# Performance work log

Measured on AMD Instinct MI355X. Metric: run time of the kernel, lower is better.

The kernel has to match this reference:

```python
import jax, jax.numpy as jnp
import numpy as np

B = 8          # batch
RES = 64       # resolution (H = W)
DIM = 512      # channels
HEADS = 8
HD = DIM // HEADS   # 64
HSP, WSP = RES, 8   # idx=0: H_sp=resolution, W_sp=split_size
NH, NW = RES // HSP, RES // WSP   # windows per axis


def setup_inputs() -> dict:
    key = jax.random.key(0)
    k1, k2, k3 = jax.random.split(key, 3)
    qkv = jax.random.normal(k1, (3, B, RES * RES, DIM), dtype=jnp.float32)
    lepe_w = jax.random.normal(k2, (DIM, 1, 3, 3), dtype=jnp.float32) * 0.1
    lepe_b = jax.random.normal(k3, (DIM,), dtype=jnp.float32) * 0.1
    return {"qkv": qkv, "lepe_w": lepe_w, "lepe_b": lepe_b}


def _to_windows(t):
    # [B, L, C] row-major -> [B*NH*NW, HSP*WSP, C]; equivalent to the
    # block-diagonal flex_attention mask grouping (y//H_sp, x//W_sp).
    t = t.reshape(B, NH, HSP, NW, WSP, DIM)
    return t.transpose(0, 1, 3, 2, 4, 5).reshape(B * NH * NW, HSP * WSP, DIM)


def _from_windows(t):
    t = t.reshape(B, NH, NW, HSP, WSP, DIM).transpose(0, 1, 3, 2, 4, 5)
    return t.reshape(B, RES * RES, DIM)


def reference(qkv, lepe_w, lepe_b):
    q, k, v = qkv[0], qkv[1], qkv[2]            # each [B, L, C]
    qw, kw, vw = _to_windows(q), _to_windows(k), _to_windows(v)

    # LePE: depthwise 3x3 conv on v laid out per-window as [n, C, HSP, WSP]
    vimg = vw.transpose(0, 2, 1).reshape(-1, DIM, HSP, WSP)
    lepe = jax.lax.conv_general_dilated(
        vimg, lepe_w, window_strides=(1, 1), padding='SAME',
        dimension_numbers=('NCHW', 'OIHW', 'NCHW'), feature_group_count=DIM)
    lepe = lepe + lepe_b[None, :, None, None]
    lepe = lepe.reshape(-1, DIM, HSP * WSP).transpose(0, 2, 1)  # [n, T, C]

    def split_heads(t):
        return t.reshape(t.shape[0], t.shape[1], HEADS, HD)

    qh, kh, vh, lh = map(split_heads, (qw, kw, vw, lepe))
    scale = 1.0 / np.sqrt(HD).astype(np.float32)  # flex_attention default scale
    scores = jnp.einsum('wqhd,wkhd->whqk', qh, kh) * scale
    attn = jax.nn.softmax(scores, axis=-1)
    out = jnp.einsum('whqk,wkhd->wqhd', attn, vh) + lh   # [n, T, H, hd]
    out = out.reshape(out.shape[0], out.shape[1], DIM)
    return _from_windows(out)
```

## Files before the change

kernel.cpp:

```cpp
#include <hip/hip_runtime.h>
#include <hip/hip_bf16.h>

#define DIMV 512
#define HDV  64
#define VSTR 520
#define VT_BASE 65536
#define SMEM_B (VT_BASE + 64 * VSTR * 2)

typedef __bf16 bf16x8_t __attribute__((ext_vector_type(8)));
typedef float f32x4_t __attribute__((ext_vector_type(4)));

union Frag { bf16x8_t v; unsigned short u[8]; unsigned int w[4]; uint2 d[2]; uint4 q; };

__device__ __forceinline__ unsigned short f2bf(float f) {
  return __builtin_bit_cast(unsigned short, (__bf16)f);
}
__device__ __forceinline__ float bf2f(unsigned int h) {
  return __builtin_bit_cast(float, h << 16);
}

__global__ __launch_bounds__(1024, 1)
void lepe_attn_kernel(const float* __restrict__ qkv,
                      const float* __restrict__ lw,
                      const float* __restrict__ lb,
                      float* __restrict__ out)
{
  __shared__ __align__(16) unsigned char smem[SMEM_B];

  const int head = blockIdx.x & 7;
  const int win  = blockIdx.x >> 3;
  const int bat  = win >> 3;
  const int nw   = win & 7;

  const int tid  = threadIdx.x;
  const int wave = tid >> 6, lane = tid & 63;
  const int l15  = lane & 15, g = lane >> 4;

  const float* qptr = qkv;
  const float* kptr = qkv + 16777216;
  const float* vptr = qkv + 33554432;
  const int rowbase = bat * 4096;

  auto growf = [&](int tok) -> size_t {
    return ((size_t)(rowbase + ((tok >> 3) << 6) + (nw << 3) + (tok & 7))) * DIMV
           + head * HDV;
  };

  const int s_t = tid >> 4;
  const int s_c = (tid & 15) * 4;
  const size_t TSTRIDE = 262144;

  const float* kg = kptr + growf(s_t) + s_c;
  const float* vg = vptr + growf(s_t) + s_c;
  const int kwbase = s_t * 128 + ((s_c * 2) ^ ((s_t & 7) << 4));

  float4 kin[8], vin[8];
  #pragma unroll
  for (int j = 0; j < 8; ++j) kin[j] = *(const float4*)(kg + (size_t)j * TSTRIDE);
  #pragma unroll
  for (int j = 0; j < 8; ++j) vin[j] = *(const float4*)(vg + (size_t)j * TSTRIDE);

  unsigned short* vt = (unsigned short*)(smem + VT_BASE);
  #pragma unroll
  for (int j = 0; j < 8; ++j) {
    uint2 kp;
    kp.x = (unsigned)f2bf(kin[j].x) | ((unsigned)f2bf(kin[j].y) << 16);
    kp.y = (unsigned)f2bf(kin[j].z) | ((unsigned)f2bf(kin[j].w) << 16);
    *(uint2*)(smem + kwbase + j * 8192) = kp;
    int t = s_t + 64 * j;
    vt[(s_c + 0) * VSTR + t] = f2bf(vin[j].x);
    vt[(s_c + 1) * VSTR + t] = f2bf(vin[j].y);
    vt[(s_c + 2) * VSTR + t] = f2bf(vin[j].z);
    vt[(s_c + 3) * VSTR + t] = f2bf(vin[j].w);
  }

  const float QSC = 0.1803368801f;
  const int qbase = wave * 32;
  Frag qf[2][2];
  #pragma unroll
  for (int qi = 0; qi < 2; ++qi) {
    const float* qp = qptr + growf(qbase + qi * 16 + l15);
    #pragma unroll
    for (int kc = 0; kc < 2; ++kc) {
      float4 f0 = *(const float4*)(qp + kc * 32 + 8 * g);
      float4 f1 = *(const float4*)(qp + kc * 32 + 8 * g + 4);
      qf[qi][kc].u[0] = f2bf(f0.x * QSC); qf[qi][kc].u[1] = f2bf(f0.y * QSC);
      qf[qi][kc].u[2] = f2bf(f0.z * QSC); qf[qi][kc].u[3] = f2bf(f0.w * QSC);
      qf[qi][kc].u[4] = f2bf(f1.x * QSC); qf[qi][kc].u[5] = f2bf(f1.y * QSC);
      qf[qi][kc].u[6] = f2bf(f1.z * QSC); qf[qi][kc].u[7] = f2bf(f1.w * QSC);
    }
  }

  __syncthreads();

  const f32x4_t zero4 = {0.f, 0.f, 0.f, 0.f};
  f32x4_t ot[4][2];
  #pragma unroll
  for (int di = 0; di < 4; ++di)
    #pragma unroll
    for (int qi = 0; qi < 2; ++qi) ot[di][qi] = zero4;
  float lsum[2] = {0.f, 0.f};

  const int ksw = (l15 & 7) << 4;
  #pragma unroll 4
  for (int kt = 0; kt < 16; ++kt) {
    Frag kf[2][2];
    #pragma unroll
    for (int ki = 0; ki < 2; ++ki) {
      const unsigned char* rowp = smem + (kt * 32 + ki * 16 + l15) * 128;
      #pragma unroll
      for (int kc = 0; kc < 2; ++kc)
        kf[ki][kc].q = *(const uint4*)(rowp + ((kc * 64 + g * 16) ^ ksw));
    }

    f32x4_t st[2][2];
    #pragma unroll
    for (int ki = 0; ki < 2; ++ki)
      #pragma unroll
      for (int qi = 0; qi < 2; ++qi) st[ki][qi] = zero4;

    __builtin_amdgcn_s_setprio(1);
    #pragma unroll
    for (int kc = 0; kc < 2; ++kc)
      #pragma unroll
      for (int ki = 0; ki < 2; ++ki)
        #pragma unroll
        for (int qi = 0; qi < 2; ++qi)
          st[ki][qi] = __builtin_amdgcn_mfma_f32_16x16x32_bf16(
              kf[ki][kc].v, qf[qi][kc].v, st[ki][qi], 0, 0, 0);
    __builtin_amdgcn_s_setprio(0);

    #pragma unroll
    for (int ki = 0; ki < 2; ++ki)
      #pragma unroll
      for (int qi = 0; qi < 2; ++qi) {
        f32x4_t s = st[ki][qi];
        #pragma unroll
        for (int r = 0; r < 4; ++r) {
          float p = __builtin_amdgcn_exp2f(s[r]);
          s[r] = p;
          lsum[qi] += p;
        }
        st[ki][qi] = s;
      }

    Frag vf[4];
    #pragma unroll
    for (int di = 0; di < 4; ++di) {
      const unsigned char* p = smem + VT_BASE + (di * 16 + l15) * (VSTR * 2)
                               + kt * 64 + 8 * g;
      vf[di].d[0] = *(const uint2*)(p);
      vf[di].d[1] = *(const uint2*)(p + 32);
    }

    __builtin_amdgcn_s_setprio(1);
    #pragma unroll
    for (int qi = 0; qi < 2; ++qi) {
      Frag pb;
      #pragma unroll
      for (int r = 0; r < 4; ++r) {
        pb.u[r]     = f2bf(st[0][qi][r]);
        pb.u[4 + r] = f2bf(st[1][qi][r]);
      }
      #pragma unroll
      for (int di = 0; di < 4; ++di)
        ot[di][qi] = __builtin_amdgcn_mfma_f32_16x16x32_bf16(
            vf[di].v, pb.v, ot[di][qi], 0, 0, 0);
    }
    __builtin_amdgcn_s_setprio(0);
  }

  float rl[2];
  #pragma unroll
  for (int qi = 0; qi < 2; ++qi) {
    float s = lsum[qi];
    s += __shfl_xor(s, 16, 64);
    s += __shfl_xor(s, 32, 64);
    rl[qi] = 1.0f / s;
  }

  float wgt[9];
  {
    const float* wp = lw + (size_t)(head * HDV + lane) * 9;
    #pragma unroll
    for (int i = 0; i < 9; ++i) wgt[i] = wp[i];
  }
  const float bias = lb[head * HDV + lane];
  const int yb = wave * 4;

  float rm[8], rc[8], rp2[8], lout[32];
  auto loadrow = [&](int y, float* dst) {
    if ((unsigned)y < 64u) {
      const unsigned char* p = smem + VT_BASE + lane * (VSTR * 2) + y * 16;
      unsigned a0 = *(const unsigned*)(p);
      unsigned a1 = *(const unsigned*)(p + 4);
      unsigned a2 = *(const unsigned*)(p + 8);
      unsigned a3 = *(const unsigned*)(p + 12);
      dst[0] = bf2f(a0 & 0xffffu); dst[1] = bf2f(a0 >> 16);
      dst[2] = bf2f(a1 & 0xffffu); dst[3] = bf2f(a1 >> 16);
      dst[4] = bf2f(a2 & 0xffffu); dst[5] = bf2f(a2 >> 16);
      dst[6] = bf2f(a3 & 0xffffu); dst[7] = bf2f(a3 >> 16);
    } else {
      #pragma unroll
      for (int x = 0; x < 8; ++x) dst[x] = 0.f;
    }
  };
  loadrow(yb - 1, rm);
  loadrow(yb, rc);
  #pragma unroll
  for (int yy = 0; yy < 4; ++yy) {
    loadrow(yb + yy + 1, rp2);
    #pragma unroll
    for (int x = 0; x < 8; ++x) {
      float acc = bias;
      if (x > 0) acc += rm[x-1]*wgt[0] + rc[x-1]*wgt[3] + rp2[x-1]*wgt[6];
      acc += rm[x]*wgt[1] + rc[x]*wgt[4] + rp2[x]*wgt[7];
      if (x < 7) acc += rm[x+1]*wgt[2] + rc[x+1]*wgt[5] + rp2[x+1]*wgt[8];
      lout[yy * 8 + x] = acc;
    }
    #pragma unroll
    for (int x = 0; x < 8; ++x) { rm[x] = rc[x]; rc[x] = rp2[x]; }
  }

  __syncthreads();

  unsigned char* bp = smem + wave * 4352;
  #pragma unroll
  for (int t = 0; t < 32; ++t)
    *(unsigned short*)(bp + t * 136 + 2 * lane) = f2bf(lout[t]);
  __syncthreads();

  #pragma unroll
  for (int qi = 0; qi < 2; ++qi) {
    const float rlq = rl[qi];
    const int tl = qi * 16 + l15;
    float* op = out + growf(qbase + tl);
    #pragma unroll
    for (int di = 0; di < 4; ++di) {
      uint2 lv = *(const uint2*)(bp + tl * 136 + di * 32 + 8 * g);
      float4 o;
      o.x = ot[di][qi][0] * rlq + bf2f(lv.x & 0xffffu);
      o.y = ot[di][qi][1] * rlq + bf2f(lv.x >> 16);
      o.z = ot[di][qi][2] * rlq + bf2f(lv.y & 0xffffu);
      o.w = ot[di][qi][3] * rlq + bf2f(lv.y >> 16);
      *(float4*)(op + di * 16 + 4 * g) = o;
    }
  }
}

extern "C" void kernel_launch(void* const* d_in, const int* in_sizes, int n_in,
                              void* d_out, int out_size, void* d_ws, size_t ws_size,
                              hipStream_t stream) {
  const float* qkv = (const float*)d_in[0];
  const float* lw  = (const float*)d_in[1];
  const float* lb  = (const float*)d_in[2];
  float* out = (float*)d_out;
  (void)in_sizes; (void)n_in; (void)out_size; (void)d_ws; (void)ws_size;

  dim3 grid(512);
  dim3 block(1024);
  hipLaunchKernelGGL(lepe_attn_kernel, grid, block, 0, stream, qkv, lw, lb, out);
}
```

Baseline: 79.97 us.

## Stream K/V loads in chunks overlapped with attention compute

```diff
diff --git a/kernel.cpp b/kernel.cpp
--- a/kernel.cpp
+++ b/kernel.cpp
@@ -3,7 +3,7 @@
 
 #define DIMV 512
 #define HDV  64
-#define VSTR 520
+#define VSTR 524
 #define VT_BASE 65536
 #define SMEM_B (VT_BASE + 64 * VSTR * 2)
 
@@ -19,7 +19,9 @@
   return __builtin_bit_cast(float, h << 16);
 }
 
-__global__ __launch_bounds__(1024, 1)
+#define BARRIER_NODRAIN() asm volatile("s_waitcnt lgkmcnt(0)\n\ts_barrier" ::: "memory")
+
+__global__ __launch_bounds__(1024, 4)
 void lepe_attn_kernel(const float* __restrict__ qkv,
                       const float* __restrict__ lw,
                       const float* __restrict__ lb,
@@ -53,45 +55,66 @@
   const float* kg = kptr + growf(s_t) + s_c;
   const float* vg = vptr + growf(s_t) + s_c;
   const int kwbase = s_t * 128 + ((s_c * 2) ^ ((s_t & 7) << 4));
-
-  float4 kin[8], vin[8];
-  #pragma unroll
-  for (int j = 0; j < 8; ++j) kin[j] = *(const float4*)(kg + (size_t)j * TSTRIDE);
-  #pragma unroll
-  for (int j = 0; j < 8; ++j) vin[j] = *(const float4*)(vg + (size_t)j * TSTRIDE);
-
   unsigned short* vt = (unsigned short*)(smem + VT_BASE);
-  #pragma unroll
-  for (int j = 0; j < 8; ++j) {
+
+  float4 ck0, ck1, cv0, cv1;
+
+  auto issue_chunk = [&](int c) {
+    ck0 = *(const float4*)(kg + (size_t)(2 * c) * TSTRIDE);
+    ck1 = *(const float4*)(kg + (size_t)(2 * c + 1) * TSTRIDE);
+    cv0 = *(const float4*)(vg + (size_t)(2 * c) * TSTRIDE);
+    cv1 = *(const float4*)(vg + (size_t)(2 * c + 1) * TSTRIDE);
+  };
+  auto write_chunk = [&](int c) {
     uint2 kp;
-    kp.x = (unsigned)f2bf(kin[j].x) | ((unsigned)f2bf(kin[j].y) << 16);
-    kp.y = (unsigned)f2bf(kin[j].z) | ((unsigned)f2bf(kin[j].w) << 16);
-    *(uint2*)(smem + kwbase + j * 8192) = kp;
-    int t = s_t + 64 * j;
-    vt[(s_c + 0) * VSTR + t] = f2bf(vin[j].x);
-    vt[(s_c + 1) * VSTR + t] = f2bf(vin[j].y);
-    vt[(s_c + 2) * VSTR + t] = f2bf(vin[j].z);
-    vt[(s_c + 3) * VSTR + t] = f2bf(vin[j].w);
-  }
-
-  const float QSC = 0.1803368801f;
+    kp.x = (unsigned)f2bf(ck0.x) | ((unsigned)f2bf(ck0.y) << 16);
+    kp.y = (unsigned)f2bf(ck0.z) | ((unsigned)f2bf(ck0.w) << 16);
+    *(uint2*)(smem + kwbase + (2 * c) * 8192) = kp;
+    kp.x = (unsigned)f2bf(ck1.x) | ((unsigned)f2bf(ck1.y) << 16);
+    kp.y = (unsigned)f2bf(ck1.z) | ((unsigned)f2bf(ck1.w) << 16);
+    *(uint2*)(smem + kwbase + (2 * c + 1) * 8192) = kp;
+    int t0 = s_t + 64 * (2 * c);
+    vt[(s_c + 0) * VSTR + t0] = f2bf(cv0.x);
+    vt[(s_c + 1) * VSTR + t0] = f2bf(cv0.y);
+    vt[(s_c + 2) * VSTR + t0] = f2bf(cv0.z);
+    vt[(s_c + 3) * VSTR + t0] = f2bf(cv0.w);
+    int t1 = t0 + 64;
+    vt[(s_c + 0) * VSTR + t1] = f2bf(cv1.x);
+    vt[(s_c + 1) * VSTR + t1] = f2bf(cv1.y);
+    vt[(s_c + 2) * VSTR + t1] = f2bf(cv1.z);
+    vt[(s_c + 3) * VSTR + t1] = f2bf(cv1.w);
+  };
+
+  issue_chunk(0);
+
   const int qbase = wave * 32;
-  Frag qf[2][2];
+  float4 qin[8];
   #pragma unroll
   for (int qi = 0; qi < 2; ++qi) {
     const float* qp = qptr + growf(qbase + qi * 16 + l15);
     #pragma unroll
     for (int kc = 0; kc < 2; ++kc) {
-      float4 f0 = *(const float4*)(qp + kc * 32 + 8 * g);
-      float4 f1 = *(const float4*)(qp + kc * 32 + 8 * g + 4);
+      qin[qi * 4 + kc * 2 + 0] = *(const float4*)(qp + kc * 32 + 8 * g);
+      qin[qi * 4 + kc * 2 + 1] = *(const float4*)(qp + kc * 32 + 8 * g + 4);
+    }
+  }
+
+  write_chunk(0);
+  BARRIER_NODRAIN();
+
+  const float QSC = 0.1803368801f;
+  Frag qf[2][2];
+  #pragma unroll
+  for (int qi = 0; qi < 2; ++qi)
+    #pragma unroll
+    for (int kc = 0; kc < 2; ++kc) {
+      const float4 f0 = qin[qi * 4 + kc * 2 + 0];
+      const float4 f1 = qin[qi * 4 + kc * 2 + 1];
       qf[qi][kc].u[0] = f2bf(f0.x * QSC); qf[qi][kc].u[1] = f2bf(f0.y * QSC);
       qf[qi][kc].u[2] = f2bf(f0.z * QSC); qf[qi][kc].u[3] = f2bf(f0.w * QSC);
       qf[qi][kc].u[4] = f2bf(f1.x * QSC); qf[qi][kc].u[5] = f2bf(f1.y * QSC);
       qf[qi][kc].u[6] = f2bf(f1.z * QSC); qf[qi][kc].u[7] = f2bf(f1.w * QSC);
     }
-  }
-
-  __syncthreads();
 
   const f32x4_t zero4 = {0.f, 0.f, 0.f, 0.f};
   f32x4_t ot[4][2];
@@ -102,72 +125,84 @@
   float lsum[2] = {0.f, 0.f};
 
   const int ksw = (l15 & 7) << 4;
-  #pragma unroll 4
-  for (int kt = 0; kt < 16; ++kt) {
-    Frag kf[2][2];
-    #pragma unroll
-    for (int ki = 0; ki < 2; ++ki) {
-      const unsigned char* rowp = smem + (kt * 32 + ki * 16 + l15) * 128;
+  #pragma unroll
+  for (int c = 0; c < 4; ++c) {
+    if (c < 3) issue_chunk(c + 1);
+
+    #pragma unroll
+    for (int t4 = 0; t4 < 4; ++t4) {
+      const int kt = c * 4 + t4;
+
+      Frag kf[2][2];
+      #pragma unroll
+      for (int ki = 0; ki < 2; ++ki) {
+        const unsigned char* rowp = smem + (kt * 32 + ki * 16 + l15) * 128;
+        #pragma unroll
+        for (int kc = 0; kc < 2; ++kc)
+          kf[ki][kc].q = *(const uint4*)(rowp + ((kc * 64 + g * 16) ^ ksw));
+      }
+
+      f32x4_t st[2][2];
+      #pragma unroll
+      for (int ki = 0; ki < 2; ++ki)
+        #pragma unroll
+        for (int qi = 0; qi < 2; ++qi) st[ki][qi] = zero4;
+
+      __builtin_amdgcn_s_setprio(1);
       #pragma unroll
       for (int kc = 0; kc < 2; ++kc)
-        kf[ki][kc].q = *(const uint4*)(rowp + ((kc * 64 + g * 16) ^ ksw));
-    }
-
-    f32x4_t st[2][2];
-    #pragma unroll
-    for (int ki = 0; ki < 2; ++ki)
-      #pragma unroll
-      for (int qi = 0; qi < 2; ++qi) st[ki][qi] = zero4;
-
-    __builtin_amdgcn_s_setprio(1);
-    #pragma unroll
-    for (int kc = 0; kc < 2; ++kc)
+        #pragma unroll
+        for (int ki = 0; ki < 2; ++ki)
+          #pragma unroll
+          for (int qi = 0; qi < 2; ++qi)
+            st[ki][qi] = __builtin_amdgcn_mfma_f32_16x16x32_bf16(
+                kf[ki][kc].v, qf[qi][kc].v, st[ki][qi], 0, 0, 0);
+      __builtin_amdgcn_s_setprio(0);
+
       #pragma unroll
       for (int ki = 0; ki < 2; ++ki)
         #pragma unroll
-        for (int qi = 0; qi < 2; ++qi)
-          st[ki][qi] = __builtin_amdgcn_mfma_f32_16x16x32_bf16(
-              kf[ki][kc].v, qf[qi][kc].v, st[ki][qi], 0, 0, 0);
-    __builtin_amdgcn_s_setprio(0);
-
-    #pragma unroll
-    for (int ki = 0; ki < 2; ++ki)
+        for (int qi = 0; qi < 2; ++qi) {
+          f32x4_t s = st[ki][qi];
+          #pragma unroll
+          for (int r = 0; r < 4; ++r) {
+            float p = __builtin_amdgcn_exp2f(s[r]);
+            s[r] = p;
+            lsum[qi] += p;
+          }
+          st[ki][qi] = s;
+        }
+
+      Frag vf[4];
+      #pragma unroll
+      for (int di = 0; di < 4; ++di) {
+        const unsigned char* p = smem + VT_BASE + (di * 16 + l15) * (VSTR * 2)
+                                 + kt * 64 + 8 * g;
+        vf[di].d[0] = *(const uint2*)(p);
+        vf[di].d[1] = *(const uint2*)(p + 32);
+      }
+
+      __builtin_amdgcn_s_setprio(1);
       #pragma unroll
       for (int qi = 0; qi < 2; ++qi) {
-        f32x4_t s = st[ki][qi];
+        Frag pb;
         #pragma unroll
         for (int r = 0; r < 4; ++r) {
-          float p = __builtin_amdgcn_exp2f(s[r]);
-          s[r] = p;
-          lsum[qi] += p;
+          pb.u[r]     = f2bf(st[0][qi][r]);
+          pb.u[4 + r] = f2bf(st[1][qi][r]);
         }
-        st[ki][qi] = s;
+        #pragma unroll
+        for (int di = 0; di < 4; ++di)
+          ot[di][qi] = __builtin_amdgcn_mfma_f32_16x16x32_bf16(
+              vf[di].v, pb.v, ot[di][qi], 0, 0, 0);
       }
-
-    Frag vf[4];
-    #pragma unroll
-    for (int di = 0; di < 4; ++di) {
-      const unsigned char* p = smem + VT_BASE + (di * 16 + l15) * (VSTR * 2)
-                               + kt * 64 + 8 * g;
-      vf[di].d[0] = *(const uint2*)(p);
-      vf[di].d[1] = *(const uint2*)(p + 32);
-    }
-
-    __builtin_amdgcn_s_setprio(1);
-    #pragma unroll
-    for (int qi = 0; qi < 2; ++qi) {
-      Frag pb;
-      #pragma unroll
-      for (int r = 0; r < 4; ++r) {
-        pb.u[r]     = f2bf(st[0][qi][r]);
-        pb.u[4 + r] = f2bf(st[1][qi][r]);
-      }
-      #pragma unroll
-      for (int di = 0; di < 4; ++di)
-        ot[di][qi] = __builtin_amdgcn_mfma_f32_16x16x32_bf16(
-            vf[di].v, pb.v, ot[di][qi], 0, 0, 0);
-    }
-    __builtin_amdgcn_s_setprio(0);
+      __builtin_amdgcn_s_setprio(0);
+    }
+
+    if (c < 3) {
+      write_chunk(c + 1);
+      BARRIER_NODRAIN();
+    }
   }
 
   float rl[2];
```

After: 78.45 us. About the same (-1.9%).
